# Kernel tuning notes

Hardware: AMD Instinct MI355X
Metric: run time of the kernel (lower is better)

The kernel has to match this reference:

```python
import jax, jax.numpy as jnp
import numpy as np

T, C, H, W = 4, 512, 14, 14
NH, HD, N = 8, 64, H * W  # heads, head_dim, tokens
EPS = 1e-5
SG_ALPHA = 4.0  # spikingjelly default sigmoid surrogate alpha


@jax.custom_vjp
def heaviside_sg(u):
    return (u >= 0.0).astype(u.dtype)

def _hs_fwd(u):
    return heaviside_sg(u), u

def _hs_bwd(u, g):
    s = jax.nn.sigmoid(SG_ALPHA * u)
    return (g * SG_ALPHA * s * (1.0 - s),)

heaviside_sg.defvjp(_hs_fwd, _hs_bwd)


def lif(x, tau=2.0, v_th=1.0):
    """Multi-step LIF over leading time dim; hard reset to 0, detach_reset."""
    def step(v, xt):
        v = v + (xt - v) / tau
        s = heaviside_sg(v - v_th)
        v = v * (1.0 - jax.lax.stop_gradient(s))
        return v, s
    _, spikes = jax.lax.scan(step, jnp.zeros_like(x[0]), x)
    return spikes


def conv1x1_bn(x, w, gamma, beta, mean, var, bias=None):
    # x: [T,C,H,W]; 1x1 conv == channel matmul, then eval-mode BN
    y = jnp.einsum('tchw,oc->tohw', x, w)
    if bias is not None:
        y = y + bias[None, :, None, None]
    scale = gamma / jnp.sqrt(var + EPS)
    return y * scale[None, :, None, None] + (beta - mean * scale)[None, :, None, None]


def to_heads(y):
    # [T,C,H,W] -> [T, NH, N, HD]
    return y.reshape(T, C, N).transpose(0, 2, 1).reshape(T, N, NH, HD).transpose(0, 2, 1, 3)


def setup_inputs() -> dict:
    key = jax.random.key(0)
    ks = jax.random.split(key, 6)
    d = {
        'x': jax.random.normal(ks[0], (T, C, H, W), jnp.float32),
        'q_w': jax.random.normal(ks[1], (C, C), jnp.float32) * 0.05,
        'k_w': jax.random.normal(ks[2], (C, C), jnp.float32) * 0.05,
        'v_w': jax.random.normal(ks[3], (C, C), jnp.float32) * 0.05,
        'proj_w': jax.random.normal(ks[4], (C, C), jnp.float32) * 0.05,
        'proj_b': jnp.zeros((C,), jnp.float32),
    }
    for p in ('q', 'k', 'v', 'proj'):
        d[p + '_gamma'] = jnp.ones((C,), jnp.float32)
        d[p + '_beta'] = jnp.zeros((C,), jnp.float32)
        d[p + '_mean'] = jnp.zeros((C,), jnp.float32)
        d[p + '_var'] = jnp.ones((C,), jnp.float32)
    return d


def reference(x, q_w, q_gamma, q_beta, q_mean, q_var,
              k_w, k_gamma, k_beta, k_mean, k_var,
              v_w, v_gamma, v_beta, v_mean, v_var,
              proj_w, proj_b, proj_gamma, proj_beta, proj_mean, proj_var):
    identity = x
    xs = lif(x)  # shortcut_lif

    q = to_heads(lif(conv1x1_bn(xs, q_w, q_gamma, q_beta, q_mean, q_var)))  # [T,NH,N,HD]
    k = to_heads(lif(conv1x1_bn(xs, k_w, k_gamma, k_beta, k_mean, k_var)))
    v = to_heads(lif(conv1x1_bn(xs, v_w, v_gamma, v_beta, v_mean, v_var)))

    kv = (k * v).sum(axis=2, keepdims=True)        # [T,NH,1,HD] linear attention reduce
    kv = lif(kv, v_th=0.5)                          # talking_heads_lif
    attn = q * kv                                   # [T,NH,N,HD]

    y = attn.transpose(0, 1, 3, 2).reshape(T, C, H, W)
    out = conv1x1_bn(y, proj_w, proj_gamma, proj_beta, proj_mean, proj_var, bias=proj_b)
    return out + identity
```

## Files before the change

### kernel.cpp

```cpp
#include <hip/hip_runtime.h>


#define TT 4
#define CC 512
#define NN 196
#define BEPS 1e-5f

#define WQT_OFF 0
#define WKT_OFF (512 * 512)
#define WVT_OFF (2 * 512 * 512)
#define WPT_OFF (3 * 512 * 512)
#define KV_OFF  (4 * 512 * 512)
#define SQ_OFF  (4 * 512 * 512 + 2048)

__global__ __launch_bounds__(256) void k0_prep(
    const float* __restrict__ qw, const float* __restrict__ kw,
    const float* __restrict__ vw, const float* __restrict__ pw,
    float* __restrict__ ws)
{
    __shared__ float tile[64][65];
    const int b   = blockIdx.x;
    const int mat = b >> 6;
    const int t6  = b & 63;
    const int to  = (t6 >> 3) * 64;
    const int tc  = (t6 & 7) * 64;
    const float* W = (mat == 0) ? qw : (mat == 1) ? kw : (mat == 2) ? vw : pw;
    float* Wt = ws + (size_t)mat * (512 * 512);
    const int lr = threadIdx.x >> 6;
    const int lc = threadIdx.x & 63;
#pragma unroll
    for (int i = 0; i < 16; ++i) {
        int r = i * 4 + lr;
        tile[r][lc] = W[(size_t)(to + r) * 512 + (tc + lc)];
    }
    __syncthreads();
#pragma unroll
    for (int i = 0; i < 16; ++i) {
        int r = i * 4 + lr;
        Wt[(size_t)(tc + r) * 512 + (to + lc)] = tile[lc][r];
    }
    if (b == 0) {
        for (int i = threadIdx.x; i < TT * CC; i += 256) ws[KV_OFF + i] = 0.0f;
    }
}

__device__ __forceinline__ int bn_lif4(const float* acc, float sc, float of, float vth) {
    float v = 0.0f;
    int bits = 0;
#pragma unroll
    for (int t = 0; t < TT; ++t) {
        float y = acc[t] * sc + of;
        v = v + (y - v) * 0.5f;
        if (v >= vth) { bits |= (1 << t); v = 0.0f; }
    }
    return bits;
}

__device__ __forceinline__ void compact_append(int flag, int ch, int lane,
                                               unsigned short* actrow, int* cntp)
{
    unsigned long long m = __ballot(flag);
    int base = 0;
    if (lane == 0 && m) base = atomicAdd(cntp, __popcll(m));
    base = __shfl(base, 0);
    if (flag) actrow[base + __popcll(m & ((1ull << lane) - 1ull))] = (unsigned short)ch;
}

__global__ __launch_bounds__(256) void ka_qkv(
    const float* __restrict__ x, float* __restrict__ ws,
    const float* __restrict__ qg, const float* __restrict__ qb,
    const float* __restrict__ qm, const float* __restrict__ qv,
    const float* __restrict__ kg, const float* __restrict__ kb,
    const float* __restrict__ km, const float* __restrict__ kvv,
    const float* __restrict__ vg, const float* __restrict__ vb,
    const float* __restrict__ vm, const float* __restrict__ vvv)
{
    const int n    = blockIdx.x;
    const int tid  = threadIdx.x;
    const int lane = tid & 63;
    const int wave = tid >> 6;
    __shared__ unsigned short act[TT][CC];
    __shared__ int cnt[TT];
    if (tid < TT) cnt[tid] = 0;
    __syncthreads();

    int xf0 = 0, xf1 = 0;
    {
        float v0 = 0.0f, v1 = 0.0f;
#pragma unroll
        for (int t = 0; t < TT; ++t) {
            float a0 = x[(size_t)(t * CC + tid) * NN + n];
            float a1 = x[(size_t)(t * CC + tid + 256) * NN + n];
            v0 = v0 + (a0 - v0) * 0.5f;
            v1 = v1 + (a1 - v1) * 0.5f;
            if (v0 >= 1.0f) { xf0 |= (1 << t); v0 = 0.0f; }
            if (v1 >= 1.0f) { xf1 |= (1 << t); v1 = 0.0f; }
        }
    }
#pragma unroll
    for (int t = 0; t < TT; ++t) {
        compact_append((xf0 >> t) & 1, tid,       lane, act[t], &cnt[t]);
        compact_append((xf1 >> t) & 1, tid + 256, lane, act[t], &cnt[t]);
    }
    __syncthreads();

    float aq0[TT] = {0,0,0,0}, aq1[TT] = {0,0,0,0};
    float ak0[TT] = {0,0,0,0}, ak1[TT] = {0,0,0,0};
    float av0[TT] = {0,0,0,0}, av1[TT] = {0,0,0,0};
    const float* Wqt = ws + WQT_OFF;
    const float* Wkt = ws + WKT_OFF;
    const float* Wvt = ws + WVT_OFF;
#pragma unroll
    for (int t = 0; t < TT; ++t) {
        const int ct = cnt[t];
        for (int i = 0; i < ct; ++i) {
            const int c = act[t][i];
            const float* rq = Wqt + (size_t)c * CC;
            const float* rk = Wkt + (size_t)c * CC;
            const float* rv = Wvt + (size_t)c * CC;
            aq0[t] += rq[tid]; aq1[t] += rq[tid + 256];
            ak0[t] += rk[tid]; ak1[t] += rk[tid + 256];
            av0[t] += rv[tid]; av1[t] += rv[tid + 256];
        }
    }

    int sqb0, sqb1, skb0, skb1, svb0, svb1;
    {
        float sc = qg[tid] / sqrtf(qv[tid] + BEPS);
        sqb0 = bn_lif4(aq0, sc, qb[tid] - qm[tid] * sc, 1.0f);
        sc = qg[tid + 256] / sqrtf(qv[tid + 256] + BEPS);
        sqb1 = bn_lif4(aq1, sc, qb[tid + 256] - qm[tid + 256] * sc, 1.0f);
        sc = kg[tid] / sqrtf(kvv[tid] + BEPS);
        skb0 = bn_lif4(ak0, sc, kb[tid] - km[tid] * sc, 1.0f);
        sc = kg[tid + 256] / sqrtf(kvv[tid + 256] + BEPS);
        skb1 = bn_lif4(ak1, sc, kb[tid + 256] - km[tid + 256] * sc, 1.0f);
        sc = vg[tid] / sqrtf(vvv[tid] + BEPS);
        svb0 = bn_lif4(av0, sc, vb[tid] - vm[tid] * sc, 1.0f);
        sc = vg[tid + 256] / sqrtf(vvv[tid + 256] + BEPS);
        svb1 = bn_lif4(av1, sc, vb[tid + 256] - vm[tid + 256] * sc, 1.0f);
    }

    unsigned* sqg = (unsigned*)(ws + SQ_OFF);
    float* kvsum = ws + KV_OFF;
#pragma unroll
    for (int t = 0; t < TT; ++t) {
        unsigned long long m = __ballot((sqb0 >> t) & 1);
        if (lane == 0) {
            sqg[((size_t)t * NN + n) * 16 + wave * 2]     = (unsigned)(m & 0xffffffffULL);
            sqg[((size_t)t * NN + n) * 16 + wave * 2 + 1] = (unsigned)(m >> 32);
        }
        m = __ballot((sqb1 >> t) & 1);
        if (lane == 0) {
            sqg[((size_t)t * NN + n) * 16 + 8 + wave * 2]     = (unsigned)(m & 0xffffffffULL);
            sqg[((size_t)t * NN + n) * 16 + 8 + wave * 2 + 1] = (unsigned)(m >> 32);
        }
        if (((skb0 >> t) & 1) && ((svb0 >> t) & 1)) atomicAdd(&kvsum[t * CC + tid], 1.0f);
        if (((skb1 >> t) & 1) && ((svb1 >> t) & 1)) atomicAdd(&kvsum[t * CC + tid + 256], 1.0f);
    }
}

__global__ __launch_bounds__(256) void kb_proj(
    const float* __restrict__ x, const float* __restrict__ ws,
    const float* __restrict__ pbias,
    const float* __restrict__ pg, const float* __restrict__ pb,
    const float* __restrict__ pm, const float* __restrict__ pv,
    float* __restrict__ out)
{
    const int n    = blockIdx.x;
    const int tid  = threadIdx.x;
    const int lane = tid & 63;
    __shared__ unsigned short act[TT][CC];
    __shared__ int cnt[TT];
    if (tid < TT) cnt[tid] = 0;
    __syncthreads();

    const float* kvsum = ws + KV_OFF;
    const unsigned* sqg = (const unsigned*)(ws + SQ_OFF);

    int f0 = 0, f1 = 0;
    {
        float v0 = 0.0f, v1 = 0.0f;
#pragma unroll
        for (int t = 0; t < TT; ++t) {
            float a0 = kvsum[t * CC + tid];
            float a1 = kvsum[t * CC + tid + 256];
            v0 = v0 + (a0 - v0) * 0.5f;
            v1 = v1 + (a1 - v1) * 0.5f;
            const int s0 = (v0 >= 0.5f), s1 = (v1 >= 0.5f);
            if (s0) v0 = 0.0f;
            if (s1) v1 = 0.0f;
            const unsigned w0 = sqg[((size_t)t * NN + n) * 16 + (tid >> 5)];
            const unsigned w1 = sqg[((size_t)t * NN + n) * 16 + 8 + (tid >> 5)];
            if (s0 && ((w0 >> (tid & 31)) & 1)) f0 |= (1 << t);
            if (s1 && ((w1 >> (tid & 31)) & 1)) f1 |= (1 << t);
        }
    }
#pragma unroll
    for (int t = 0; t < TT; ++t) {
        compact_append((f0 >> t) & 1, tid,       lane, act[t], &cnt[t]);
        compact_append((f1 >> t) & 1, tid + 256, lane, act[t], &cnt[t]);
    }
    __syncthreads();

    float a0[TT] = {0,0,0,0}, a1[TT] = {0,0,0,0};
    const float* Wpt = ws + WPT_OFF;
#pragma unroll
    for (int t = 0; t < TT; ++t) {
        const int ct = cnt[t];
        for (int i = 0; i < ct; ++i) {
            const int c = act[t][i];
            const float* r = Wpt + (size_t)c * CC;
            a0[t] += r[tid];
            a1[t] += r[tid + 256];
        }
    }

    {
        const float sc0 = pg[tid] / sqrtf(pv[tid] + BEPS);
        const float of0 = pb[tid] - pm[tid] * sc0;
        const float bi0 = pbias[tid];
        const float sc1 = pg[tid + 256] / sqrtf(pv[tid + 256] + BEPS);
        const float of1 = pb[tid + 256] - pm[tid + 256] * sc1;
        const float bi1 = pbias[tid + 256];
#pragma unroll
        for (int t = 0; t < TT; ++t) {
            const size_t i0 = (size_t)(t * CC + tid) * NN + n;
            const size_t i1 = (size_t)(t * CC + tid + 256) * NN + n;
            out[i0] = (a0[t] + bi0) * sc0 + of0 + x[i0];
            out[i1] = (a1[t] + bi1) * sc1 + of1 + x[i1];
        }
    }
}

extern "C" void kernel_launch(void* const* d_in, const int* in_sizes, int n_in,
                              void* d_out, int out_size, void* d_ws, size_t ws_size,
                              hipStream_t stream) {
    const float* x     = (const float*)d_in[0];
    const float* qw    = (const float*)d_in[1];
    const float* kw    = (const float*)d_in[2];
    const float* vw    = (const float*)d_in[3];
    const float* pw    = (const float*)d_in[4];
    const float* pbias = (const float*)d_in[5];
    const float* qg = (const float*)d_in[6],  *qb = (const float*)d_in[7];
    const float* qm = (const float*)d_in[8],  *qv = (const float*)d_in[9];
    const float* kg = (const float*)d_in[10], *kb = (const float*)d_in[11];
    const float* km = (const float*)d_in[12], *kv = (const float*)d_in[13];
    const float* vg = (const float*)d_in[14], *vb = (const float*)d_in[15];
    const float* vm = (const float*)d_in[16], *vv = (const float*)d_in[17];
    const float* pg = (const float*)d_in[18], *pb = (const float*)d_in[19];
    const float* pm = (const float*)d_in[20], *pv = (const float*)d_in[21];
    float* ws  = (float*)d_ws;
    float* out = (float*)d_out;

    hipLaunchKernelGGL(k0_prep, dim3(256), dim3(256), 0, stream, qw, kw, vw, pw, ws);
    hipLaunchKernelGGL(ka_qkv, dim3(196), dim3(256), 0, stream, x, ws,
                       qg, qb, qm, qv, kg, kb, km, kv, vg, vb, vm, vv);
    hipLaunchKernelGGL(kb_proj, dim3(196), dim3(256), 0, stream, x, ws,
                       pbias, pg, pb, pm, pv, out);
}
```

Measured before the change: 124.1 us.

## Split spike-sparse GEMMs across output halves with precomputed active lists and transposed epilogue

```diff
diff --git a/kernel.cpp b/kernel.cpp
--- a/kernel.cpp
+++ b/kernel.cpp
@@ -7,40 +7,106 @@
 #define BEPS 1e-5f
 
 #define WQT_OFF 0
-#define WKT_OFF (512 * 512)
-#define WVT_OFF (2 * 512 * 512)
-#define WPT_OFF (3 * 512 * 512)
-#define KV_OFF  (4 * 512 * 512)
-#define SQ_OFF  (4 * 512 * 512 + 2048)
+#define WKT_OFF (513 * 512)
+#define WVT_OFF (2 * 513 * 512)
+#define WPT_OFF (3 * 513 * 512)
+#define KV_OFF  (4 * 513 * 512)
+#define SQ_OFF  (KV_OFF + 2048)
+#define ACT_OFF (SQ_OFF + 12544)
+#define CNT_OFF (ACT_OFF + 200704)
+#define OT_OFF  (CNT_OFF + 784)
 
 __global__ __launch_bounds__(256) void k0_prep(
     const float* __restrict__ qw, const float* __restrict__ kw,
     const float* __restrict__ vw, const float* __restrict__ pw,
-    float* __restrict__ ws)
+    const float* __restrict__ x, float* __restrict__ ws)
 {
-    __shared__ float tile[64][65];
     const int b   = blockIdx.x;
-    const int mat = b >> 6;
-    const int t6  = b & 63;
-    const int to  = (t6 >> 3) * 64;
-    const int tc  = (t6 & 7) * 64;
-    const float* W = (mat == 0) ? qw : (mat == 1) ? kw : (mat == 2) ? vw : pw;
-    float* Wt = ws + (size_t)mat * (512 * 512);
-    const int lr = threadIdx.x >> 6;
-    const int lc = threadIdx.x & 63;
-#pragma unroll
-    for (int i = 0; i < 16; ++i) {
-        int r = i * 4 + lr;
-        tile[r][lc] = W[(size_t)(to + r) * 512 + (tc + lc)];
+    const int tid = threadIdx.x;
+
+    if (b < 256) {
+        __shared__ float tile[64][65];
+        const int mat = b >> 6;
+        const int t6  = b & 63;
+        const int to  = (t6 >> 3) * 64;
+        const int tc  = (t6 & 7) * 64;
+        const float* W = (mat == 0) ? qw : (mat == 1) ? kw : (mat == 2) ? vw : pw;
+        float* Wt = ws + (size_t)mat * (513 * 512);
+        const int lr = tid >> 6;
+        const int lc = tid & 63;
+#pragma unroll
+        for (int i = 0; i < 16; ++i) {
+            int r = i * 4 + lr;
+            tile[r][lc] = W[(size_t)(to + r) * 512 + (tc + lc)];
+        }
+        __syncthreads();
+#pragma unroll
+        for (int i = 0; i < 16; ++i) {
+            int r = i * 4 + lr;
+            Wt[(size_t)(tc + r) * 512 + (to + lc)] = tile[lc][r];
+        }
+        if (t6 == 0) {
+            for (int i = tid; i < 512; i += 256) Wt[(size_t)512 * 512 + i] = 0.0f;
+        }
+        if (b == 0) {
+            for (int i = tid; i < TT * CC; i += 256) ws[KV_OFF + i] = 0.0f;
+        }
+        return;
+    }
+
+    const int n    = b - 256;
+    const int lane = tid & 63;
+    const int wave = tid >> 6;
+    __shared__ unsigned long long msk[TT][8];
+
+    int xf0 = 0, xf1 = 0;
+    {
+        float v0 = 0.0f, v1 = 0.0f;
+#pragma unroll
+        for (int t = 0; t < TT; ++t) {
+            float a0 = x[(size_t)(t * CC + tid) * NN + n];
+            float a1 = x[(size_t)(t * CC + tid + 256) * NN + n];
+            v0 = v0 + (a0 - v0) * 0.5f;
+            v1 = v1 + (a1 - v1) * 0.5f;
+            if (v0 >= 1.0f) { xf0 |= (1 << t); v0 = 0.0f; }
+            if (v1 >= 1.0f) { xf1 |= (1 << t); v1 = 0.0f; }
+        }
+    }
+#pragma unroll
+    for (int t = 0; t < TT; ++t) {
+        unsigned long long m0 = __ballot((xf0 >> t) & 1);
+        unsigned long long m1 = __ballot((xf1 >> t) & 1);
+        if (lane == 0) { msk[t][wave] = m0; msk[t][4 + wave] = m1; }
     }
     __syncthreads();
-#pragma unroll
-    for (int i = 0; i < 16; ++i) {
-        int r = i * 4 + lr;
-        Wt[(size_t)(tc + r) * 512 + (to + lc)] = tile[lc][r];
-    }
-    if (b == 0) {
-        for (int i = threadIdx.x; i < TT * CC; i += 256) ws[KV_OFF + i] = 0.0f;
+
+    unsigned short* actg = (unsigned short*)(ws + ACT_OFF);
+    int* cntg = (int*)(ws + CNT_OFF);
+    const unsigned long long ltm = (1ull << lane) - 1ull;
+#pragma unroll
+    for (int t = 0; t < TT; ++t) {
+        unsigned short* row = actg + ((size_t)t * NN + n) * 512;
+        if ((xf0 >> t) & 1) {
+            int base = 0;
+            for (int s2 = 0; s2 < wave; ++s2) base += __popcll(msk[t][s2]);
+            base += __popcll(msk[t][wave] & ltm);
+            row[base] = (unsigned short)tid;
+        }
+        if ((xf1 >> t) & 1) {
+            int base = 0;
+            for (int s2 = 0; s2 < 4 + wave; ++s2) base += __popcll(msk[t][s2]);
+            base += __popcll(msk[t][4 + wave] & ltm);
+            row[base] = (unsigned short)(tid + 256);
+        }
+    }
+    if (tid < TT) {
+        int tot = 0;
+#pragma unroll
+        for (int s2 = 0; s2 < 8; ++s2) tot += __popcll(msk[tid][s2]);
+        int totp = (tot + 7) & ~7;
+        unsigned short* row = actg + ((size_t)tid * NN + n) * 512;
+        for (int i = tot; i < totp; ++i) row[i] = 512;
+        cntg[tid * NN + n] = totp;
     }
 }
 
@@ -56,18 +122,8 @@
     return bits;
 }
 
-__device__ __forceinline__ void compact_append(int flag, int ch, int lane,
-                                               unsigned short* actrow, int* cntp)
-{
-    unsigned long long m = __ballot(flag);
-    int base = 0;
-    if (lane == 0 && m) base = atomicAdd(cntp, __popcll(m));
-    base = __shfl(base, 0);
-    if (flag) actrow[base + __popcll(m & ((1ull << lane) - 1ull))] = (unsigned short)ch;
-}
-
 __global__ __launch_bounds__(256) void ka_qkv(
-    const float* __restrict__ x, float* __restrict__ ws,
+    float* __restrict__ ws,
     const float* __restrict__ qg, const float* __restrict__ qb,
     const float* __restrict__ qm, const float* __restrict__ qv,
     const float* __restrict__ kg, const float* __restrict__ kb,
@@ -75,104 +131,84 @@
     const float* __restrict__ vg, const float* __restrict__ vb,
     const float* __restrict__ vm, const float* __restrict__ vvv)
 {
-    const int n    = blockIdx.x;
+    const int bx   = blockIdx.x;
+    const int n    = bx >> 1;
+    const int s    = bx & 1;
     const int tid  = threadIdx.x;
     const int lane = tid & 63;
     const int wave = tid >> 6;
-    __shared__ unsigned short act[TT][CC];
-    __shared__ int cnt[TT];
-    if (tid < TT) cnt[tid] = 0;
-    __syncthreads();
-
-    int xf0 = 0, xf1 = 0;
-    {
-        float v0 = 0.0f, v1 = 0.0f;
-#pragma unroll
-        for (int t = 0; t < TT; ++t) {
-            float a0 = x[(size_t)(t * CC + tid) * NN + n];
-            float a1 = x[(size_t)(t * CC + tid + 256) * NN + n];
-            v0 = v0 + (a0 - v0) * 0.5f;
-            v1 = v1 + (a1 - v1) * 0.5f;
-            if (v0 >= 1.0f) { xf0 |= (1 << t); v0 = 0.0f; }
-            if (v1 >= 1.0f) { xf1 |= (1 << t); v1 = 0.0f; }
-        }
-    }
-#pragma unroll
-    for (int t = 0; t < TT; ++t) {
-        compact_append((xf0 >> t) & 1, tid,       lane, act[t], &cnt[t]);
-        compact_append((xf1 >> t) & 1, tid + 256, lane, act[t], &cnt[t]);
-    }
-    __syncthreads();
-
-    float aq0[TT] = {0,0,0,0}, aq1[TT] = {0,0,0,0};
-    float ak0[TT] = {0,0,0,0}, ak1[TT] = {0,0,0,0};
-    float av0[TT] = {0,0,0,0}, av1[TT] = {0,0,0,0};
+    const int o    = s * 256 + tid;
+
     const float* Wqt = ws + WQT_OFF;
     const float* Wkt = ws + WKT_OFF;
     const float* Wvt = ws + WVT_OFF;
-#pragma unroll
-    for (int t = 0; t < TT; ++t) {
-        const int ct = cnt[t];
-        for (int i = 0; i < ct; ++i) {
-            const int c = act[t][i];
-            const float* rq = Wqt + (size_t)c * CC;
-            const float* rk = Wkt + (size_t)c * CC;
-            const float* rv = Wvt + (size_t)c * CC;
-            aq0[t] += rq[tid]; aq1[t] += rq[tid + 256];
-            ak0[t] += rk[tid]; ak1[t] += rk[tid + 256];
-            av0[t] += rv[tid]; av1[t] += rv[tid + 256];
-        }
-    }
-
-    int sqb0, sqb1, skb0, skb1, svb0, svb1;
+    const unsigned short* actg = (const unsigned short*)(ws + ACT_OFF);
+    const int* cntg = (const int*)(ws + CNT_OFF);
+
+    float aq[TT] = {0,0,0,0}, ak[TT] = {0,0,0,0}, av[TT] = {0,0,0,0};
+#pragma unroll
+    for (int t = 0; t < TT; ++t) {
+        const int ctp = cntg[t * NN + n];
+        const unsigned short* lp = actg + ((size_t)t * NN + n) * 512;
+        for (int i = 0; i < ctp; i += 8) {
+            const uint4 cc = *(const uint4*)(lp + i);
+            int cs[8];
+            cs[0] = cc.x & 0xffff; cs[1] = cc.x >> 16;
+            cs[2] = cc.y & 0xffff; cs[3] = cc.y >> 16;
+            cs[4] = cc.z & 0xffff; cs[5] = cc.z >> 16;
+            cs[6] = cc.w & 0xffff; cs[7] = cc.w >> 16;
+#pragma unroll
+            for (int j = 0; j < 8; ++j) {
+                const int c = __builtin_amdgcn_readfirstlane(cs[j]);
+                const size_t rb = (size_t)c * 512;
+                aq[t] += Wqt[rb + o];
+                ak[t] += Wkt[rb + o];
+                av[t] += Wvt[rb + o];
+            }
+        }
+    }
+
+    int sqb, skb, svb;
     {
-        float sc = qg[tid] / sqrtf(qv[tid] + BEPS);
-        sqb0 = bn_lif4(aq0, sc, qb[tid] - qm[tid] * sc, 1.0f);
-        sc = qg[tid + 256] / sqrtf(qv[tid + 256] + BEPS);
-        sqb1 = bn_lif4(aq1, sc, qb[tid + 256] - qm[tid + 256] * sc, 1.0f);
-        sc = kg[tid] / sqrtf(kvv[tid] + BEPS);
-        skb0 = bn_lif4(ak0, sc, kb[tid] - km[tid] * sc, 1.0f);
-        sc = kg[tid + 256] / sqrtf(kvv[tid + 256] + BEPS);
-        skb1 = bn_lif4(ak1, sc, kb[tid + 256] - km[tid + 256] * sc, 1.0f);
-        sc = vg[tid] / sqrtf(vvv[tid] + BEPS);
-        svb0 = bn_lif4(av0, sc, vb[tid] - vm[tid] * sc, 1.0f);
-        sc = vg[tid + 256] / sqrtf(vvv[tid + 256] + BEPS);
-        svb1 = bn_lif4(av1, sc, vb[tid + 256] - vm[tid + 256] * sc, 1.0f);
+        float sc = qg[o] / sqrtf(qv[o] + BEPS);
+        sqb = bn_lif4(aq, sc, qb[o] - qm[o] * sc, 1.0f);
+        sc = kg[o] / sqrtf(kvv[o] + BEPS);
+        skb = bn_lif4(ak, sc, kb[o] - km[o] * sc, 1.0f);
+        sc = vg[o] / sqrtf(vvv[o] + BEPS);
+        svb = bn_lif4(av, sc, vb[o] - vm[o] * sc, 1.0f);
     }
 
     unsigned* sqg = (unsigned*)(ws + SQ_OFF);
     float* kvsum = ws + KV_OFF;
 #pragma unroll
     for (int t = 0; t < TT; ++t) {
-        unsigned long long m = __ballot((sqb0 >> t) & 1);
+        unsigned long long m = __ballot((sqb >> t) & 1);
         if (lane == 0) {
-            sqg[((size_t)t * NN + n) * 16 + wave * 2]     = (unsigned)(m & 0xffffffffULL);
-            sqg[((size_t)t * NN + n) * 16 + wave * 2 + 1] = (unsigned)(m >> 32);
-        }
-        m = __ballot((sqb1 >> t) & 1);
-        if (lane == 0) {
-            sqg[((size_t)t * NN + n) * 16 + 8 + wave * 2]     = (unsigned)(m & 0xffffffffULL);
-            sqg[((size_t)t * NN + n) * 16 + 8 + wave * 2 + 1] = (unsigned)(m >> 32);
-        }
-        if (((skb0 >> t) & 1) && ((svb0 >> t) & 1)) atomicAdd(&kvsum[t * CC + tid], 1.0f);
-        if (((skb1 >> t) & 1) && ((svb1 >> t) & 1)) atomicAdd(&kvsum[t * CC + tid + 256], 1.0f);
+            sqg[((size_t)t * NN + n) * 16 + s * 8 + wave * 2]     = (unsigned)(m & 0xffffffffULL);
+            sqg[((size_t)t * NN + n) * 16 + s * 8 + wave * 2 + 1] = (unsigned)(m >> 32);
+        }
+        if (((skb >> t) & 1) & ((svb >> t) & 1)) atomicAdd(&kvsum[t * CC + o], 1.0f);
     }
 }
 
 __global__ __launch_bounds__(256) void kb_proj(
-    const float* __restrict__ x, const float* __restrict__ ws,
+    const float* __restrict__ ws,
     const float* __restrict__ pbias,
     const float* __restrict__ pg, const float* __restrict__ pb,
     const float* __restrict__ pm, const float* __restrict__ pv,
-    float* __restrict__ out)
+    float* __restrict__ wso)
 {
-    const int n    = blockIdx.x;
+    const int bx   = blockIdx.x;
+    const int n    = bx >> 1;
+    const int s    = bx & 1;
     const int tid  = threadIdx.x;
     const int lane = tid & 63;
-    __shared__ unsigned short act[TT][CC];
-    __shared__ int cnt[TT];
-    if (tid < TT) cnt[tid] = 0;
-    __syncthreads();
+    const int wave = tid >> 6;
+    const int o    = s * 256 + tid;
+
+    __shared__ unsigned long long msk[TT][8];
+    __shared__ __align__(16) unsigned short lst[TT][520];
+    __shared__ int cntp[TT];
 
     const float* kvsum = ws + KV_OFF;
     const unsigned* sqg = (const unsigned*)(ws + SQ_OFF);
@@ -197,37 +233,98 @@
     }
 #pragma unroll
     for (int t = 0; t < TT; ++t) {
-        compact_append((f0 >> t) & 1, tid,       lane, act[t], &cnt[t]);
-        compact_append((f1 >> t) & 1, tid + 256, lane, act[t], &cnt[t]);
+        unsigned long long m0 = __ballot((f0 >> t) & 1);
+        unsigned long long m1 = __ballot((f1 >> t) & 1);
+        if (lane == 0) { msk[t][wave] = m0; msk[t][4 + wave] = m1; }
     }
     __syncthreads();
 
-    float a0[TT] = {0,0,0,0}, a1[TT] = {0,0,0,0};
+    const unsigned long long ltm = (1ull << lane) - 1ull;
+#pragma unroll
+    for (int t = 0; t < TT; ++t) {
+        if ((f0 >> t) & 1) {
+            int base = 0;
+            for (int s2 = 0; s2 < wave; ++s2) base += __popcll(msk[t][s2]);
+            base += __popcll(msk[t][wave] & ltm);
+            lst[t][base] = (unsigned short)tid;
+        }
+        if ((f1 >> t) & 1) {
+            int base = 0;
+            for (int s2 = 0; s2 < 4 + wave; ++s2) base += __popcll(msk[t][s2]);
+            base += __popcll(msk[t][4 + wave] & ltm);
+            lst[t][base] = (unsigned short)(tid + 256);
+        }
+    }
+    if (tid < TT) {
+        int tot = 0;
+#pragma unroll
+        for (int s2 = 0; s2 < 8; ++s2) tot += __popcll(msk[tid][s2]);
+        int totp = (tot + 7) & ~7;
+        for (int i = tot; i < totp; ++i) lst[tid][i] = 512;
+        cntp[tid] = totp;
+    }
+    __syncthreads();
+
+    float a[TT] = {0,0,0,0};
     const float* Wpt = ws + WPT_OFF;
 #pragma unroll
     for (int t = 0; t < TT; ++t) {
-        const int ct = cnt[t];
-        for (int i = 0; i < ct; ++i) {
-            const int c = act[t][i];
-            const float* r = Wpt + (size_t)c * CC;
-            a0[t] += r[tid];
-            a1[t] += r[tid + 256];
+        const int ct = cntp[t];
+        for (int i = 0; i < ct; i += 8) {
+            const uint4 cc = *(const uint4*)(&lst[t][i]);
+            int cs[8];
+            cs[0] = cc.x & 0xffff; cs[1] = cc.x >> 16;
+            cs[2] = cc.y & 0xffff; cs[3] = cc.y >> 16;
+            cs[4] = cc.z & 0xffff; cs[5] = cc.z >> 16;
+            cs[6] = cc.w & 0xffff; cs[7] = cc.w >> 16;
+#pragma unroll
+            for (int j = 0; j < 8; ++j) {
+                const int c = __builtin_amdgcn_readfirstlane(cs[j]);
+                a[t] += Wpt[(size_t)c * 512 + o];
+            }
         }
     }
 
     {
-        const float sc0 = pg[tid] / sqrtf(pv[tid] + BEPS);
-        const float of0 = pb[tid] - pm[tid] * sc0;
-        const float bi0 = pbias[tid];
-        const float sc1 = pg[tid + 256] / sqrtf(pv[tid + 256] + BEPS);
-        const float of1 = pb[tid + 256] - pm[tid + 256] * sc1;
-        const float bi1 = pbias[tid + 256];
+        const float sc = pg[o] / sqrtf(pv[o] + BEPS);
+        const float of = pb[o] - pm[o] * sc;
+        const float bi = pbias[o];
+        float* outT = wso;
 #pragma unroll
         for (int t = 0; t < TT; ++t) {
-            const size_t i0 = (size_t)(t * CC + tid) * NN + n;
-            const size_t i1 = (size_t)(t * CC + tid + 256) * NN + n;
-            out[i0] = (a0[t] + bi0) * sc0 + of0 + x[i0];
-            out[i1] = (a1[t] + bi1) * sc1 + of1 + x[i1];
+            outT[((size_t)t * NN + n) * CC + o] = (a[t] + bi) * sc + of;
+        }
+    }
+}
+
+__global__ __launch_bounds__(256) void k2_out(
+    const float* __restrict__ x, const float* __restrict__ ws,
+    float* __restrict__ out)
+{
+    __shared__ float tile[64][65];
+    const int b   = blockIdx.x;
+    const int t   = b >> 5;
+    const int ct  = (b >> 2) & 7;
+    const int nt  = b & 3;
+    const int c0  = ct * 64;
+    const int n0  = nt * 64;
+    const int tid = threadIdx.x;
+    const int lr  = tid >> 6;
+    const int lc  = tid & 63;
+    const float* outT = ws + OT_OFF;
+#pragma unroll
+    for (int i = 0; i < 16; ++i) {
+        int r = i * 4 + lr;
+        if (n0 + r < NN)
+            tile[r][lc] = outT[((size_t)t * NN + (n0 + r)) * CC + c0 + lc];
+    }
+    __syncthreads();
+#pragma unroll
+    for (int i = 0; i < 16; ++i) {
+        int r = i * 4 + lr;
+        if (n0 + lc < NN) {
+            const size_t gi = ((size_t)t * CC + (c0 + r)) * NN + n0 + lc;
+            out[gi] = tile[lc][r] + x[gi];
         }
     }
 }
@@ -252,9 +349,11 @@
     float* ws  = (float*)d_ws;
     float* out = (float*)d_out;
 
-    hipLaunchKernelGGL(k0_prep, dim3(256), dim3(256), 0, stream, qw, kw, vw, pw, ws);
-    hipLaunchKernelGGL(ka_qkv, dim3(196), dim3(256), 0, stream, x, ws,
+    hipLaunchKernelGGL(k0_prep, dim3(256 + NN), dim3(256), 0, stream,
+                       qw, kw, vw, pw, x, ws);
+    hipLaunchKernelGGL(ka_qkv, dim3(2 * NN), dim3(256), 0, stream, ws,
                        qg, qb, qm, qv, kg, kb, km, kv, vg, vb, vm, vv);
-    hipLaunchKernelGGL(kb_proj, dim3(196), dim3(256), 0, stream, x, ws,
-                       pbias, pg, pb, pm, pv, out);
-}
+    hipLaunchKernelGGL(kb_proj, dim3(2 * NN), dim3(256), 0, stream, ws,
+                       pbias, pg, pb, pm, pv, ws + OT_OFF);
+    hipLaunchKernelGGL(k2_out, dim3(128), dim3(256), 0, stream, x, ws, out);
+}
```

Result: slower. 127.7 us (+2.9%).
